# Performance work log

Measured on AMD Instinct MI355X. Metric: run time of the kernel, lower is better.

## Reference

```python
import jax, jax.numpy as jnp
import numpy as np

FIX_SCALE = np.array([[0.,0.,0.],[1.,0.,0.],[0.,1.,0.],[0.,0.,1.],[-1.,0.,0.],[0.,-1.,0.]], dtype=np.float32)
NUM_HEADS = 8
ATTN_DIMS = 512
HEAD_DIMS = ATTN_DIMS // NUM_HEADS
NUM_LEARN = 6
SIG_CLAMP = 9.21  # safe_sigmoid clamp


def quat_to_rotmat(q):
    # q: [G,4] (w,x,y,z), normalized -> [G,3,3]
    q = q / jnp.linalg.norm(q, axis=-1, keepdims=True)
    w, x, y, z = q[..., 0], q[..., 1], q[..., 2], q[..., 3]
    r0 = jnp.stack([1 - 2*(y*y + z*z), 2*(x*y - w*z), 2*(x*z + w*y)], -1)
    r1 = jnp.stack([2*(x*y + w*z), 1 - 2*(x*x + z*z), 2*(y*z - w*x)], -1)
    r2 = jnp.stack([2*(x*z - w*y), 2*(y*z + w*x), 1 - 2*(x*x + y*y)], -1)
    return jnp.stack([r0, r1, r2], -2)


def bilinear_sample(fm, gx, gy):
    # fm: [C,H,W]; gx,gy: [...] in [-1,1]; align_corners=False, zero padding
    C, H, W = fm.shape
    x = (gx + 1.0) * (W * 0.5) - 0.5
    y = (gy + 1.0) * (H * 0.5) - 0.5
    x0 = jnp.floor(x); y0 = jnp.floor(y)
    wx1 = x - x0; wx0 = 1.0 - wx1
    wy1 = y - y0; wy0 = 1.0 - wy1

    def gather(xf, yf):
        xi = xf.astype(jnp.int32); yi = yf.astype(jnp.int32)
        valid = (xi >= 0) & (xi < W) & (yi >= 0) & (yi < H)
        xi = jnp.clip(xi, 0, W - 1); yi = jnp.clip(yi, 0, H - 1)
        return fm[:, yi, xi] * valid[None].astype(fm.dtype)  # [C, ...]

    out = (gather(x0, y0) * (wx0 * wy0)[None]
           + gather(x0 + 1, y0) * (wx1 * wy0)[None]
           + gather(x0, y0 + 1) * (wx0 * wy1)[None]
           + gather(x0 + 1, y0 + 1) * (wx1 * wy1)[None])
    return jnp.moveaxis(out, 0, -1)  # [..., C]


def setup_inputs() -> dict:
    key = jax.random.key(0)
    ks = jax.random.split(key, 16)
    G, BS, GFD = 8192, 1, 32
    means = jax.random.uniform(ks[0], (G, 3), minval=-1.0, maxval=1.0)
    means = means.at[:, 2].add(3.0)  # push in front of camera
    scales = jax.random.uniform(ks[1], (G, 3), minval=0.01, maxval=0.1)
    rotations = jax.random.normal(ks[2], (G, 4))
    features = jax.random.normal(ks[3], (BS, G, 3, GFD))
    transforms = jnp.tile(jnp.eye(4)[None], (G, 1, 1)) + 0.01 * jax.random.normal(ks[4], (G, 4, 4))
    f = 64.0
    proj = jnp.array([[f, 0., 32., 0.], [0., f, 32., 0.], [0., 0., 1., 0.], [0., 0., 0., 1.]], dtype=jnp.float32)
    projection = jnp.tile(proj[None], (BS, 1, 1))
    image_features = jax.random.normal(ks[5], (BS, 256, 64, 64))
    s = lambda d: 1.0 / np.sqrt(d)
    Wq = jax.random.normal(ks[6], (GFD, ATTN_DIMS)) * s(GFD)
    Wk = jax.random.normal(ks[7], (ATTN_DIMS, 256)) * s(256)
    Wv = jax.random.normal(ks[8], (ATTN_DIMS, 256)) * s(256)
    W_off = jax.random.normal(ks[9], (HEAD_DIMS + 3, NUM_LEARN * 3)) * s(HEAD_DIMS + 3)
    b_off = jnp.zeros((NUM_LEARN * 3,))
    Wout = jax.random.normal(ks[10], (ATTN_DIMS, GFD)) * s(ATTN_DIMS)
    b_out = jnp.zeros((GFD,))
    return {"means": means, "scales": scales, "rotations": rotations, "features": features,
            "transforms": transforms, "projection": projection, "image_features": image_features,
            "Wq": Wq, "Wk": Wk, "Wv": Wv, "W_off": W_off, "b_off": b_off, "Wout": Wout, "b_out": b_out}


def reference(means, scales, rotations, features, transforms, projection, image_features,
              Wq, Wk, Wv, W_off, b_off, Wout, b_out):
    G = means.shape[0]
    bs = features.shape[0]
    H, HD = NUM_HEADS, HEAD_DIMS
    h_img, w_img = image_features.shape[-2:]

    # queries: [bs,G,3,attn] -> [bs,H,G,3,hd]
    q_full = jnp.einsum('bgtf,fa->bgta', features, Wq)
    q = q_full.reshape(bs, G, 3, H, HD).transpose(0, 3, 1, 2, 4)

    # transform means to world space with per-gaussian 4x4
    homo = jnp.concatenate([means, jnp.ones((G, 1), means.dtype)], -1)  # [G,4]
    means_w = jnp.einsum('gij,gj->gi', transforms, homo)[:, :3]  # [G,3]

    # OffsetNet: per-head learnable offsets from (world mean, token-mean query)
    q_mean = q.mean(axis=3)  # [bs,H,G,hd]
    m_b = jnp.broadcast_to(means_w[None, None], (bs, H, G, 3))
    off_in = jnp.concatenate([m_b, q_mean], -1)  # [bs,H,G,hd+3]
    learnable = jax.nn.sigmoid(jnp.clip(off_in @ W_off + b_off, -SIG_CLAMP, SIG_CLAMP))
    learnable = learnable.reshape(bs, H, G, NUM_LEARN, 3) - 0.5
    fix = jnp.broadcast_to(jnp.asarray(FIX_SCALE)[None, None, None], (bs, H, G, FIX_SCALE.shape[0], 3))
    scale_all = jnp.concatenate([fix, learnable], axis=-2)  # [bs,H,G,K,3]
    K = scale_all.shape[-2]

    offset_pts = scale_all * scales[None, None, :, None, :]
    RT = jnp.swapaxes(quat_to_rotmat(rotations), -1, -2)  # [G,3,3]
    offset_pts = jnp.einsum('gij,bhgkj->bhgki', RT, offset_pts) + means_w[None, None, :, None, :]

    # project to 2D, normalize to [0,1), then to grid coords [-1,1]
    pts4 = jnp.concatenate([offset_pts, jnp.ones_like(offset_pts[..., :1])], -1)
    p = jnp.einsum('bij,bhgkj->bhgki', projection, pts4)
    p2 = p[..., :2] / jnp.clip(p[..., 2:3], 1e-5)
    wh = jnp.array([w_img, h_img], dtype=p2.dtype)
    pnorm = jnp.clip(p2 / wh, 0.0, 0.9999)
    grid = 2.0 * pnorm - 1.0  # [bs,H,G,K,2]

    # key/value maps via 1x1 conv, split into per-head channel groups
    kmap = jnp.einsum('ac,bchw->bahw', Wk, image_features).reshape(bs, H, HD, h_img, w_img)
    vmap_ = jnp.einsum('ac,bchw->bahw', Wv, image_features).reshape(bs, H, HD, h_img, w_img)

    sample_bh = jax.vmap(jax.vmap(bilinear_sample, in_axes=(0, 0, 0)), in_axes=(0, 0, 0))
    k_s = sample_bh(kmap, grid[..., 0], grid[..., 1])   # [bs,H,G,K,hd]
    v_s = sample_bh(vmap_, grid[..., 0], grid[..., 1])  # [bs,H,G,K,hd]

    scale = HD ** -0.5
    scores = jnp.einsum('bhgid,bhgkd->bhgik', q, k_s) * scale
    attn = jax.nn.softmax(scores, axis=-1)
    out = jnp.einsum('bhgik,bhgkd->bhgid', attn, v_s)  # [bs,H,G,3,hd]
    out = out.transpose(0, 2, 3, 1, 4).reshape(bs, G, 3, H * HD)  # b g i (h d)
    out = out @ Wout + b_out
    return out + features
```

## Files before the change

kernel.cpp:

```cpp
#include <hip/hip_runtime.h>
#include <hip/hip_bf16.h>
#include <hip/hip_fp16.h>

typedef _Float16 half2v __attribute__((ext_vector_type(2)));
typedef _Float16 half8v __attribute__((ext_vector_type(8)));
typedef __attribute__((ext_vector_type(4))) float float4v;

__device__ __forceinline__ half2v u2h(unsigned u) { return __builtin_bit_cast(half2v, u); }
__device__ __forceinline__ unsigned h2u(half2v h) { return __builtin_bit_cast(unsigned, h); }
__device__ __forceinline__ unsigned short f2hu(float f) {
    _Float16 h = (_Float16)f; return __builtin_bit_cast(unsigned short, h);
}
__device__ __forceinline__ unsigned packh(float lo, float hi) {
    half2v h; h[0] = (_Float16)lo; h[1] = (_Float16)hi; return h2u(h);
}
__device__ __forceinline__ void ld8h(const unsigned short* p, float* f) {
    uint4 u = *(const uint4*)p;
    half2v h0 = u2h(u.x), h1 = u2h(u.y), h2 = u2h(u.z), h3 = u2h(u.w);
    f[0] = (float)h0[0]; f[1] = (float)h0[1]; f[2] = (float)h1[0]; f[3] = (float)h1[1];
    f[4] = (float)h2[0]; f[5] = (float)h2[1]; f[6] = (float)h3[0]; f[7] = (float)h3[1];
}

__global__ __launch_bounds__(256) void preconvert_kernel(
    const float* __restrict__ img, const float* __restrict__ Wk,
    const float* __restrict__ Wv, unsigned short* __restrict__ imgh,
    unsigned short* __restrict__ wkvh)
{
    const size_t base = ((size_t)blockIdx.x * 256 + threadIdx.x) * 4;
    float4 v;
    unsigned short* dst;
    if (base < 1048576) {
        v = *(const float4*)(img + base);
        dst = imgh + base;
    } else {
        size_t o = base - 1048576;
        v = *(const float4*)((o < 131072) ? (Wk + o) : (Wv + (o - 131072)));
        dst = wkvh + o;
    }
    *(uint2*)dst = make_uint2(packh(v.x, v.y), packh(v.z, v.w));
}

__global__ __launch_bounds__(256) void conv_f16_kernel(
    const unsigned short* __restrict__ imgh, const unsigned short* __restrict__ wkvh,
    unsigned short* __restrict__ buf)
{
    __shared__ __attribute__((aligned(16))) unsigned short Bt[64][264];
    const int tid = threadIdx.x;
    const int p0 = blockIdx.x * 64;
    const int o0 = blockIdx.y * 64;

#pragma unroll
    for (int i = 0; i < 4; i++) {
        int chunk = i * 256 + tid;
        int kp  = chunk >> 3;
        int pxg = (chunk & 7) * 8;
        uint4 r0 = *(const uint4*)(imgh + (size_t)(2 * kp) * 4096 + p0 + pxg);
        uint4 r1 = *(const uint4*)(imgh + (size_t)(2 * kp + 1) * 4096 + p0 + pxg);
        unsigned lo[8], hi[8];
        lo[0] = r0.x & 0xffffu; lo[1] = r0.x >> 16; lo[2] = r0.y & 0xffffu; lo[3] = r0.y >> 16;
        lo[4] = r0.z & 0xffffu; lo[5] = r0.z >> 16; lo[6] = r0.w & 0xffffu; lo[7] = r0.w >> 16;
        hi[0] = r1.x & 0xffffu; hi[1] = r1.x >> 16; hi[2] = r1.y & 0xffffu; hi[3] = r1.y >> 16;
        hi[4] = r1.z & 0xffffu; hi[5] = r1.z >> 16; hi[6] = r1.w & 0xffffu; hi[7] = r1.w >> 16;
#pragma unroll
        for (int j = 0; j < 8; j++)
            *(unsigned*)&Bt[pxg + j][2 * kp] = lo[j] | (hi[j] << 16);
    }
    __syncthreads();

    const int w = tid >> 6, l = tid & 63;
    const int m = l & 15, quad = l >> 4;
    const int mrow = w * 16 + m;
    const unsigned short* Wsel = wkvh + ((o0 < 512) ? 0 : 131072);
    const int obase = (o0 < 512) ? o0 : (o0 - 512);

    float4v acc[4] = {{0,0,0,0},{0,0,0,0},{0,0,0,0},{0,0,0,0}};
#pragma unroll
    for (int kk = 0; kk < 8; kk++) {
        const int kofs = kk * 32 + quad * 8;
        half8v af = *(const half8v*)&Bt[mrow][kofs];
#pragma unroll
        for (int nt = 0; nt < 4; nt++) {
            const int row = obase + nt * 16 + m;
            half8v b8 = *(const half8v*)(Wsel + (size_t)row * 256 + kofs);
            acc[nt] = __builtin_amdgcn_mfma_f32_16x16x32_f16(af, b8, acc[nt], 0, 0, 0);
        }
    }
#pragma unroll
    for (int nt = 0; nt < 4; nt++) {
#pragma unroll
        for (int r = 0; r < 4; r++) {
            size_t px = p0 + w * 16 + quad * 4 + r;
            buf[px * 1024 + o0 + nt * 16 + m] = f2hu(acc[nt][r]);
        }
    }
}

__global__ __launch_bounds__(256) void conv_mfma_kernel(
    const float* __restrict__ img, const float* __restrict__ Wk,
    const float* __restrict__ Wv, unsigned short* __restrict__ buf)
{
    __shared__ __attribute__((aligned(16))) unsigned short Bt[64][264];
    const int tid = threadIdx.x;
    const int p0 = blockIdx.x * 64;
    const int o0 = blockIdx.y * 64;

#pragma unroll
    for (int i = 0; i < 4; i++) {
        int chunk = i * 256 + tid;
        int kp  = chunk >> 3;
        int pxg = (chunk & 7) * 8;
        const float* r0 = img + (size_t)(2 * kp) * 4096 + p0 + pxg;
        const float* r1 = img + (size_t)(2 * kp + 1) * 4096 + p0 + pxg;
        float4 a0 = *(const float4*)r0, a1 = *(const float4*)(r0 + 4);
        float4 b0 = *(const float4*)r1, b1 = *(const float4*)(r1 + 4);
        unsigned lo[8], hi[8];
        lo[0] = f2hu(a0.x); lo[1] = f2hu(a0.y); lo[2] = f2hu(a0.z); lo[3] = f2hu(a0.w);
        lo[4] = f2hu(a1.x); lo[5] = f2hu(a1.y); lo[6] = f2hu(a1.z); lo[7] = f2hu(a1.w);
        hi[0] = f2hu(b0.x); hi[1] = f2hu(b0.y); hi[2] = f2hu(b0.z); hi[3] = f2hu(b0.w);
        hi[4] = f2hu(b1.x); hi[5] = f2hu(b1.y); hi[6] = f2hu(b1.z); hi[7] = f2hu(b1.w);
#pragma unroll
        for (int j = 0; j < 8; j++)
            *(unsigned*)&Bt[pxg + j][2 * kp] = lo[j] | (hi[j] << 16);
    }
    __syncthreads();

    const int w = tid >> 6, l = tid & 63;
    const int m = l & 15, quad = l >> 4;
    const int mrow = w * 16 + m;
    const float* Wsel = (o0 < 512) ? Wk : Wv;
    const int obase = (o0 < 512) ? o0 : (o0 - 512);

    float4v acc[4] = {{0,0,0,0},{0,0,0,0},{0,0,0,0},{0,0,0,0}};
#pragma unroll
    for (int kk = 0; kk < 8; kk++) {
        const int kofs = kk * 32 + quad * 8;
        half8v af = *(const half8v*)&Bt[mrow][kofs];
#pragma unroll
        for (int nt = 0; nt < 4; nt++) {
            const int row = obase + nt * 16 + m;
            const float* wp = Wsel + (size_t)row * 256 + kofs;
            float4 w0 = *(const float4*)wp, w1 = *(const float4*)(wp + 4);
            half8v b8;
            b8[0] = (_Float16)w0.x; b8[1] = (_Float16)w0.y;
            b8[2] = (_Float16)w0.z; b8[3] = (_Float16)w0.w;
            b8[4] = (_Float16)w1.x; b8[5] = (_Float16)w1.y;
            b8[6] = (_Float16)w1.z; b8[7] = (_Float16)w1.w;
            acc[nt] = __builtin_amdgcn_mfma_f32_16x16x32_f16(af, b8, acc[nt], 0, 0, 0);
        }
    }
#pragma unroll
    for (int nt = 0; nt < 4; nt++) {
#pragma unroll
        for (int r = 0; r < 4; r++) {
            size_t px = p0 + w * 16 + quad * 4 + r;
            buf[px * 1024 + o0 + nt * 16 + m] = f2hu(acc[nt][r]);
        }
    }
}

__global__ __launch_bounds__(256) void qgemm_kernel(
    const float* __restrict__ features, const float* __restrict__ Wq,
    unsigned short* __restrict__ qfull)
{
    __shared__ __attribute__((aligned(16))) unsigned short WqT[256][40];
    const int tid = threadIdx.x;
    const int R0 = blockIdx.x * 64;
    const int n0 = blockIdx.y * 256;
#pragma unroll
    for (int k = 0; k < 32; k++)
        WqT[tid][k] = f2hu(Wq[(size_t)k * 512 + n0 + tid]);
    __syncthreads();

    const int w = tid >> 6, l = tid & 63, m = l & 15, quad = l >> 4;
    const int row = R0 + w * 16 + m;
    const float* fp = features + (size_t)row * 32 + quad * 8;
    float4 f0 = *(const float4*)fp, f1 = *(const float4*)(fp + 4);
    half8v af;
    af[0] = (_Float16)f0.x; af[1] = (_Float16)f0.y;
    af[2] = (_Float16)f0.z; af[3] = (_Float16)f0.w;
    af[4] = (_Float16)f1.x; af[5] = (_Float16)f1.y;
    af[6] = (_Float16)f1.z; af[7] = (_Float16)f1.w;
    float4v acc[16];
#pragma unroll
    for (int t = 0; t < 16; t++) acc[t] = (float4v){0.f, 0.f, 0.f, 0.f};
#pragma unroll
    for (int t = 0; t < 16; t++) {
        half8v b8 = *(const half8v*)&WqT[t * 16 + m][quad * 8];
        acc[t] = __builtin_amdgcn_mfma_f32_16x16x32_f16(af, b8, acc[t], 0, 0, 0);
    }
    const int rb = R0 + w * 16 + quad * 4;
#pragma unroll
    for (int t = 0; t < 16; t++)
#pragma unroll
        for (int r = 0; r < 4; r++)
            qfull[(size_t)(rb + r) * 512 + n0 + t * 16 + m] = f2hu(acc[t][r]);
}

__global__ __launch_bounds__(256, 8) void attn_core_kernel(
    const float* __restrict__ means, const float* __restrict__ scales,
    const float* __restrict__ rot,   const float* __restrict__ transforms,
    const float* __restrict__ projection, const float* __restrict__ W_off,
    const float* __restrict__ b_off, const unsigned short* __restrict__ buf,
    unsigned short* __restrict__ qfull)
{
    __shared__ __attribute__((aligned(16))) unsigned qf2[768];
    __shared__ __attribute__((aligned(16))) unsigned vsh2[3072];
    __shared__ __attribute__((aligned(16))) float qm_u[512];
    __shared__ float lrn[144];
    __shared__ float mw[3], sc3[3], Rt[9], pr[12];

    short4* corner = (short4*)qm_u;
    float*  att    = qm_u + 192;
    float*  wofl   = (float*)vsh2;
    float*  bofl   = wofl + 1206;

    const int g = blockIdx.x, tid = threadIdx.x;

    for (int i = tid; i < 1206; i += 256) wofl[i] = W_off[i];
    if (tid < 18) bofl[tid] = b_off[tid];
    if (tid >= 32 && tid < 35) {
        sc3[tid - 32] = scales[(size_t)g * 3 + (tid - 32)];
    } else if (tid >= 36 && tid < 48) {
        pr[tid - 36] = projection[tid - 36];
    } else if (tid == 48) {
        float w = rot[(size_t)g * 4],     x = rot[(size_t)g * 4 + 1];
        float y = rot[(size_t)g * 4 + 2], z = rot[(size_t)g * 4 + 3];
        float n = rsqrtf(w * w + x * x + y * y + z * z);
        w *= n; x *= n; y *= n; z *= n;
        float R00 = 1 - 2 * (y * y + z * z), R01 = 2 * (x * y - w * z), R02 = 2 * (x * z + w * y);
        float R10 = 2 * (x * y + w * z), R11 = 1 - 2 * (x * x + z * z), R12 = 2 * (y * z - w * x);
        float R20 = 2 * (x * z - w * y), R21 = 2 * (y * z + w * x), R22 = 1 - 2 * (x * x + y * y);
        Rt[0] = R00; Rt[1] = R10; Rt[2] = R20;
        Rt[3] = R01; Rt[4] = R11; Rt[5] = R21;
        Rt[6] = R02; Rt[7] = R12; Rt[8] = R22;
    } else if (tid >= 52 && tid < 55) {
        int i = tid - 52;
        float m0 = means[(size_t)g * 3];
        float m1 = means[(size_t)g * 3 + 1];
        float m2 = means[(size_t)g * 3 + 2];
        const float* T = transforms + (size_t)g * 16 + i * 4;
        mw[i] = T[0] * m0 + T[1] * m1 + T[2] * m2 + T[3];
    }
    {
        const unsigned* qsrc = (const unsigned*)(qfull + (size_t)g * 1536);
#pragma unroll
        for (int i = 0; i < 3; i++) {
            int e = tid + i * 256;
            qf2[e] = qsrc[e];
        }
    }
    __syncthreads();

    {
        half2v a = u2h(qf2[tid]), b = u2h(qf2[256 + tid]), c = u2h(qf2[512 + tid]);
        qm_u[tid * 2]     = ((float)a[0] + (float)b[0] + (float)c[0]) * (1.f / 3.f);
        qm_u[tid * 2 + 1] = ((float)a[1] + (float)b[1] + (float)c[1]) * (1.f / 3.f);
    }
    __syncthreads();

    if (tid < 144) {
        int h = tid / 18, l = tid % 18;
        float s = bofl[l];
#pragma unroll
        for (int i = 0; i < 3; i++) s += mw[i] * wofl[i * 18 + l];
        for (int d = 0; d < 64; d++) s += qm_u[h * 64 + d] * wofl[(3 + d) * 18 + l];
        s = fminf(fmaxf(s, -9.21f), 9.21f);
        lrn[tid] = 1.f / (1.f + expf(-s)) - 0.5f;
    }
    __syncthreads();

    if (tid < 96) {
        int h = tid / 12, k = tid % 12;
        float s0, s1, s2;
        if (k < 6) {
            const float FSx[6] = {0.f, 1.f, 0.f, 0.f, -1.f, 0.f};
            const float FSy[6] = {0.f, 0.f, 1.f, 0.f, 0.f, -1.f};
            const float FSz[6] = {0.f, 0.f, 0.f, 1.f, 0.f, 0.f};
            s0 = FSx[k]; s1 = FSy[k]; s2 = FSz[k];
        } else {
            int b = h * 18 + (k - 6) * 3;
            s0 = lrn[b]; s1 = lrn[b + 1]; s2 = lrn[b + 2];
        }
        float o0 = s0 * sc3[0], o1 = s1 * sc3[1], o2 = s2 * sc3[2];
        float wx = Rt[0] * o0 + Rt[1] * o1 + Rt[2] * o2 + mw[0];
        float wy = Rt[3] * o0 + Rt[4] * o1 + Rt[5] * o2 + mw[1];
        float wz = Rt[6] * o0 + Rt[7] * o1 + Rt[8] * o2 + mw[2];
        float px = pr[0] * wx + pr[1] * wy + pr[2]  * wz + pr[3];
        float py = pr[4] * wx + pr[5] * wy + pr[6]  * wz + pr[7];
        float pz = pr[8] * wx + pr[9] * wy + pr[10] * wz + pr[11];
        pz = fmaxf(pz, 1e-5f);
        float gx = fminf(fmaxf(px / pz * (1.f / 64.f), 0.f), 0.9999f);
        float gy = fminf(fmaxf(py / pz * (1.f / 64.f), 0.f), 0.9999f);
        float x = gx * 64.f - 0.5f, y = gy * 64.f - 0.5f;
        float fx = floorf(x), fy = floorf(y);
        short4 cn;
        cn.x = (short)(int)fx;
        cn.y = (short)(int)fy;
        cn.z = (short)(unsigned short)fminf((x - fx) * 65536.f, 65535.f);
        cn.w = (short)(unsigned short)fminf((y - fy) * 65536.f, 65535.f);
        corner[tid] = cn;
    }
    __syncthreads();

    {
        const int slice = tid & 7, grp = tid >> 3;
#pragma unroll
        for (int it = 0; it < 3; it++) {
            const int p = it * 32 + grp;
            const int h = p / 12, k = p - h * 12;
            short4 cn = corner[p];
            int x0 = cn.x, y0 = cn.y, x1 = x0 + 1, y1 = y0 + 1;
            float wx1 = (float)(unsigned short)cn.z * (1.f / 65536.f);
            float wy1 = (float)(unsigned short)cn.w * (1.f / 65536.f);
            float wx0 = 1.f - wx1, wy0 = 1.f - wy1;
            bool vx0 = (unsigned)x0 < 64u, vx1 = (unsigned)x1 < 64u;
            bool vy0 = (unsigned)y0 < 64u, vy1 = (unsigned)y1 < 64u;
            int xc0 = min(max(x0, 0), 63), xc1 = min(max(x1, 0), 63);
            int yc0 = min(max(y0, 0), 63), yc1 = min(max(y1, 0), 63);
            int   off[4];
            float wt[4];
            off[0] = (yc0 * 64 + xc0) * 1024; wt[0] = (vx0 & vy0) ? wx0 * wy0 : 0.f;
            off[1] = (yc0 * 64 + xc1) * 1024; wt[1] = (vx1 & vy0) ? wx1 * wy0 : 0.f;
            off[2] = (yc1 * 64 + xc0) * 1024; wt[2] = (vx0 & vy1) ? wx0 * wy1 : 0.f;
            off[3] = (yc1 * 64 + xc1) * 1024; wt[3] = (vx1 & vy1) ? wx1 * wy1 : 0.f;
            const int a = h * 64 + slice * 8;
            const unsigned short* bp = buf + a;
            half2v ka2[4] = {{0,0},{0,0},{0,0},{0,0}};
            half2v va2[4] = {{0,0},{0,0},{0,0},{0,0}};
#pragma unroll
            for (int c = 0; c < 4; c++) {
                _Float16 wh = (_Float16)wt[c];
                half2v w2; w2[0] = wh; w2[1] = wh;
                uint4 uk = *(const uint4*)(bp + off[c]);
                uint4 uv = *(const uint4*)(bp + off[c] + 512);
                ka2[0] += w2 * u2h(uk.x); ka2[1] += w2 * u2h(uk.y);
                ka2[2] += w2 * u2h(uk.z); ka2[3] += w2 * u2h(uk.w);
                va2[0] += w2 * u2h(uv.x); va2[1] += w2 * u2h(uv.y);
                va2[2] += w2 * u2h(uv.z); va2[3] += w2 * u2h(uv.w);
            }
            const int pa = h * 32 + slice * 4;
            *(uint4*)&vsh2[p * 32 + slice * 4] =
                make_uint4(h2u(va2[0]), h2u(va2[1]), h2u(va2[2]), h2u(va2[3]));
            float sp[3];
#pragma unroll
            for (int t = 0; t < 3; t++) {
                uint4 q4 = *(const uint4*)&qf2[t * 256 + pa];
                float s = __builtin_amdgcn_fdot2(u2h(q4.x), ka2[0], 0.f, false);
                s = __builtin_amdgcn_fdot2(u2h(q4.y), ka2[1], s, false);
                s = __builtin_amdgcn_fdot2(u2h(q4.z), ka2[2], s, false);
                s = __builtin_amdgcn_fdot2(u2h(q4.w), ka2[3], s, false);
                sp[t] = s;
            }
#pragma unroll
            for (int msk = 1; msk < 8; msk <<= 1) {
#pragma unroll
                for (int t = 0; t < 3; t++) sp[t] += __shfl_xor(sp[t], msk);
            }
            if (slice == 0) {
#pragma unroll
                for (int t = 0; t < 3; t++) att[(h * 3 + t) * 12 + k] = sp[t] * 0.125f;
            }
        }
    }
    __syncthreads();

    if (tid < 24) {
        float* row = att + tid * 12;
        float m = row[0];
#pragma unroll
        for (int k = 1; k < 12; k++) m = fmaxf(m, row[k]);
        float e_[12]; float ssum = 0.f;
#pragma unroll
        for (int k = 0; k < 12; k++) { e_[k] = expf(row[k] - m); ssum += e_[k]; }
        float inv = 1.f / ssum;
#pragma unroll
        for (int k = 0; k < 12; k++) row[k] = e_[k] * inv;
    }
    __syncthreads();

    {
        unsigned* oa32 = (unsigned*)(qfull + (size_t)g * 1536);
#pragma unroll
        for (int i = 0; i < 3; i++) {
            int e = tid + i * 256;
            int t = e >> 8, a2p = e & 255;
            int h = a2p >> 5, ddp = a2p & 31;
            const float* ar = att + (h * 3 + t) * 12;
            const unsigned* vp = vsh2 + h * 12 * 32 + ddp;
            half2v acc = {0, 0};
#pragma unroll
            for (int k = 0; k < 12; k++) {
                _Float16 ah = (_Float16)ar[k];
                half2v a2; a2[0] = ah; a2[1] = ah;
                acc += a2 * u2h(vp[k * 32]);
            }
            oa32[e] = h2u(acc);
        }
    }
}

__global__ __launch_bounds__(256) void outgemm_kernel(
    const unsigned short* __restrict__ oa, const float* __restrict__ Wout,
    const float* __restrict__ b_out, const float* __restrict__ features,
    float* __restrict__ out)
{
    __shared__ __attribute__((aligned(16))) unsigned short WT[32][520];
    const int tid = threadIdx.x;
    const int R0 = blockIdx.x * 64;
#pragma unroll
    for (int j = 0; j < 64; j++) {
        int lin = j * 256 + tid;
        WT[lin & 31][lin >> 5] = f2hu(Wout[lin]);
    }
    __syncthreads();

    const int w = tid >> 6, l = tid & 63, m = l & 15, quad = l >> 4;
    const int row = R0 + w * 16 + m;
    float4v acc[2] = {{0,0,0,0},{0,0,0,0}};
#pragma unroll
    for (int kk = 0; kk < 16; kk++) {
        half8v af = *(const half8v*)(oa + (size_t)row * 512 + kk * 32 + quad * 8);
#pragma unroll
        for (int t = 0; t < 2; t++) {
            half8v b8 = *(const half8v*)&WT[t * 16 + m][kk * 32 + quad * 8];
            acc[t] = __builtin_amdgcn_mfma_f32_16x16x32_f16(af, b8, acc[t], 0, 0, 0);
        }
    }
    const int rb = R0 + w * 16 + quad * 4;
#pragma unroll
    for (int t = 0; t < 2; t++) {
        int col = t * 16 + m;
        float bb = b_out[col];
#pragma unroll
        for (int r = 0; r < 4; r++) {
            int rr = rb + r;
            out[(size_t)rr * 32 + col] = acc[t][r] + bb + features[(size_t)rr * 32 + col];
        }
    }
}

__global__ __launch_bounds__(256, 6) void attn_fused_kernel(
    const float* __restrict__ means, const float* __restrict__ scales,
    const float* __restrict__ rot,   const float* __restrict__ features,
    const float* __restrict__ transforms, const float* __restrict__ projection,
    const float* __restrict__ Wq,    const float* __restrict__ W_off,
    const float* __restrict__ b_off, const float* __restrict__ Wout,
    const float* __restrict__ b_out, const unsigned short* __restrict__ buf,
    float* __restrict__ out)
{
    __shared__ float feat[96];
    __shared__ __attribute__((aligned(16))) float qf[1536];
    __shared__ float qm[512];
    __shared__ float mw[3], sc3[3], Rt[9], pr[12];
    __shared__ float lrn[144];
    __shared__ int   coff[96][4];
    __shared__ float cwt[96][4];
    __shared__ __attribute__((aligned(16))) char pool[12288];
    __shared__ float att[288];

    unsigned short* vsh = (unsigned short*)pool;
    const int g = blockIdx.x, tid = threadIdx.x;

    if (tid < 96) {
        feat[tid] = features[(size_t)g * 96 + tid];
    } else if (tid < 99) {
        sc3[tid - 96] = scales[(size_t)g * 3 + (tid - 96)];
    } else if (tid >= 100 && tid < 112) {
        pr[tid - 100] = projection[tid - 100];
    } else if (tid == 112) {
        float w = rot[(size_t)g * 4],     x = rot[(size_t)g * 4 + 1];
        float y = rot[(size_t)g * 4 + 2], z = rot[(size_t)g * 4 + 3];
        float n = rsqrtf(w * w + x * x + y * y + z * z);
        w *= n; x *= n; y *= n; z *= n;
        float R00 = 1 - 2 * (y * y + z * z), R01 = 2 * (x * y - w * z), R02 = 2 * (x * z + w * y);
        float R10 = 2 * (x * y + w * z), R11 = 1 - 2 * (x * x + z * z), R12 = 2 * (y * z - w * x);
        float R20 = 2 * (x * z - w * y), R21 = 2 * (y * z + w * x), R22 = 1 - 2 * (x * x + y * y);
        Rt[0] = R00; Rt[1] = R10; Rt[2] = R20;
        Rt[3] = R01; Rt[4] = R11; Rt[5] = R21;
        Rt[6] = R02; Rt[7] = R12; Rt[8] = R22;
    } else if (tid >= 116 && tid < 119) {
        int i = tid - 116;
        float m0 = means[(size_t)g * 3];
        float m1 = means[(size_t)g * 3 + 1];
        float m2 = means[(size_t)g * 3 + 2];
        const float* T = transforms + (size_t)g * 16 + i * 4;
        mw[i] = T[0] * m0 + T[1] * m1 + T[2] * m2 + T[3];
    }
    __syncthreads();

    {
        const int a0 = tid * 2;
        float s00 = 0.f, s01 = 0.f, s10 = 0.f, s11 = 0.f, s20 = 0.f, s21 = 0.f;
#pragma unroll
        for (int f = 0; f < 32; f++) {
            float2 w2 = *(const float2*)(Wq + (size_t)f * 512 + a0);
            float f0 = feat[f], f1 = feat[32 + f], f2 = feat[64 + f];
            s00 += f0 * w2.x; s01 += f0 * w2.y;
            s10 += f1 * w2.x; s11 += f1 * w2.y;
            s20 += f2 * w2.x; s21 += f2 * w2.y;
        }
        *(float2*)(qf + a0)        = make_float2(s00, s01);
        *(float2*)(qf + 512 + a0)  = make_float2(s10, s11);
        *(float2*)(qf + 1024 + a0) = make_float2(s20, s21);
    }
    __syncthreads();

    qm[tid]       = (qf[tid]       + qf[tid + 512] + qf[tid + 1024]) * (1.f / 3.f);
    qm[tid + 256] = (qf[tid + 256] + qf[tid + 768] + qf[tid + 1280]) * (1.f / 3.f);
    __syncthreads();

    if (tid < 144) {
        int h = tid / 18, l = tid % 18;
        float s = b_off[l];
#pragma unroll
        for (int i = 0; i < 3; i++) s += mw[i] * W_off[i * 18 + l];
        for (int d = 0; d < 64; d++) s += qm[h * 64 + d] * W_off[(size_t)(3 + d) * 18 + l];
        s = fminf(fmaxf(s, -9.21f), 9.21f);
        lrn[tid] = 1.f / (1.f + expf(-s)) - 0.5f;
    }
    __syncthreads();

    if (tid < 96) {
        int h = tid / 12, k = tid % 12;
        float s0, s1, s2;
        if (k < 6) {
            const float FSx[6] = {0.f, 1.f, 0.f, 0.f, -1.f, 0.f};
            const float FSy[6] = {0.f, 0.f, 1.f, 0.f, 0.f, -1.f};
            const float FSz[6] = {0.f, 0.f, 0.f, 1.f, 0.f, 0.f};
            s0 = FSx[k]; s1 = FSy[k]; s2 = FSz[k];
        } else {
            int b = h * 18 + (k - 6) * 3;
            s0 = lrn[b]; s1 = lrn[b + 1]; s2 = lrn[b + 2];
        }
        float o0 = s0 * sc3[0], o1 = s1 * sc3[1], o2 = s2 * sc3[2];
        float wx = Rt[0] * o0 + Rt[1] * o1 + Rt[2] * o2 + mw[0];
        float wy = Rt[3] * o0 + Rt[4] * o1 + Rt[5] * o2 + mw[1];
        float wz = Rt[6] * o0 + Rt[7] * o1 + Rt[8] * o2 + mw[2];
        float px = pr[0] * wx + pr[1] * wy + pr[2]  * wz + pr[3];
        float py = pr[4] * wx + pr[5] * wy + pr[6]  * wz + pr[7];
        float pz = pr[8] * wx + pr[9] * wy + pr[10] * wz + pr[11];
        pz = fmaxf(pz, 1e-5f);
        float gx = fminf(fmaxf(px / pz * (1.f / 64.f), 0.f), 0.9999f);
        float gy = fminf(fmaxf(py / pz * (1.f / 64.f), 0.f), 0.9999f);
        float x = gx * 64.f - 0.5f, y = gy * 64.f - 0.5f;
        float fx = floorf(x), fy = floorf(y);
        int x0 = (int)fx, y0 = (int)fy;
        float wx1 = x - fx, wx0c = 1.f - wx1;
        float wy1 = y - fy, wy0c = 1.f - wy1;
        int xs[2] = {x0, x0 + 1}, ys[2] = {y0, y0 + 1};
        float wxs[2] = {wx0c, wx1}, wys[2] = {wy0c, wy1};
#pragma unroll
        for (int c = 0; c < 4; c++) {
            int dx = c & 1, dy = c >> 1;
            int xi = xs[dx], yi = ys[dy];
            bool v = (xi >= 0) & (xi < 64) & (yi >= 0) & (yi < 64);
            int xc = min(max(xi, 0), 63), yc = min(max(yi, 0), 63);
            coff[tid][c] = (yc * 64 + xc) * 1024;
            cwt[tid][c]  = v ? wxs[dx] * wys[dy] : 0.f;
        }
    }
    __syncthreads();

    {
        const int slice = tid & 7, d0 = slice * 8, grp = tid >> 3;
#pragma unroll
        for (int it = 0; it < 3; it++) {
            const int p = it * 32 + grp;
            const int h = p / 12, k = p - h * 12;
            const int a = h * 64 + d0;
            const unsigned short* bp = buf + a;
            float ka[8] = {0,0,0,0,0,0,0,0}, va[8] = {0,0,0,0,0,0,0,0}, t8[8];
#pragma unroll
            for (int c = 0; c < 4; c++) {
                const int   o = coff[p][c];
                const float w = cwt[p][c];
                ld8h(bp + o, t8);
#pragma unroll
                for (int j = 0; j < 8; j++) ka[j] += w * t8[j];
                ld8h(bp + o + 512, t8);
#pragma unroll
                for (int j = 0; j < 8; j++) va[j] += w * t8[j];
            }
            uint4 pv;
            pv.x = packh(va[0], va[1]); pv.y = packh(va[2], va[3]);
            pv.z = packh(va[4], va[5]); pv.w = packh(va[6], va[7]);
            *(uint4*)(vsh + p * 64 + d0) = pv;
            float sp[3];
#pragma unroll
            for (int t = 0; t < 3; t++) {
                const float* qp = qf + t * 512 + a;
                float s = 0.f;
#pragma unroll
                for (int j = 0; j < 8; j++) s += qp[j] * ka[j];
                sp[t] = s;
            }
#pragma unroll
            for (int msk = 1; msk < 8; msk <<= 1) {
#pragma unroll
                for (int t = 0; t < 3; t++) sp[t] += __shfl_xor(sp[t], msk);
            }
            if (slice == 0) {
#pragma unroll
                for (int t = 0; t < 3; t++) att[(h * 3 + t) * 12 + k] = sp[t] * 0.125f;
            }
        }
    }
    __syncthreads();

    if (tid < 24) {
        float* row = att + tid * 12;
        float m = row[0];
#pragma unroll
        for (int k = 1; k < 12; k++) m = fmaxf(m, row[k]);
        float e_[12]; float ssum = 0.f;
#pragma unroll
        for (int k = 0; k < 12; k++) { e_[k] = expf(row[k] - m); ssum += e_[k]; }
        float inv = 1.f / ssum;
#pragma unroll
        for (int k = 0; k < 12; k++) row[k] = e_[k] * inv;
    }
    __syncthreads();

#pragma unroll
    for (int i = 0; i < 6; i++) {
        int e = tid + i * 256;
        int t = e >> 9, a = e & 511, h = a >> 6, dd = a & 63;
        const float* ar = att + (h * 3 + t) * 12;
        const unsigned short* vp = vsh + (h * 12) * 64 + dd;
        float s = 0.f;
#pragma unroll
        for (int k = 0; k < 12; k++) {
            _Float16 hh = __builtin_bit_cast(_Float16, vp[k * 64]);
            s += ar[k] * (float)hh;
        }
        qf[e] = s;
    }
    __syncthreads();

    {
        float* red = (float*)pool;
        const int c0 = (tid & 15) * 2, slice = tid >> 4;
        const int abase = slice * 32;
        float a00 = 0.f, a01 = 0.f, a10 = 0.f, a11 = 0.f, a20 = 0.f, a21 = 0.f;
#pragma unroll
        for (int i = 0; i < 32; i++) {
            int a = abase + i;
            float2 w2 = *(const float2*)(Wout + (size_t)a * 32 + c0);
            float o0 = qf[a], o1 = qf[512 + a], o2 = qf[1024 + a];
            a00 += o0 * w2.x; a01 += o0 * w2.y;
            a10 += o1 * w2.x; a11 += o1 * w2.y;
            a20 += o2 * w2.x; a21 += o2 * w2.y;
        }
        __syncthreads();
        red[(slice * 3 + 0) * 32 + c0] = a00; red[(slice * 3 + 0) * 32 + c0 + 1] = a01;
        red[(slice * 3 + 1) * 32 + c0] = a10; red[(slice * 3 + 1) * 32 + c0 + 1] = a11;
        red[(slice * 3 + 2) * 32 + c0] = a20; red[(slice * 3 + 2) * 32 + c0 + 1] = a21;
        __syncthreads();
        if (tid < 96) {
            int t = tid >> 5, c = tid & 31;
            float acc = b_out[c] + feat[tid];
#pragma unroll
            for (int s = 0; s < 16; s++) acc += red[(s * 3 + t) * 32 + c];
            out[(size_t)g * 96 + tid] = acc;
        }
    }
}

extern "C" void kernel_launch(void* const* d_in, const int* in_sizes, int n_in,
                              void* d_out, int out_size, void* d_ws, size_t ws_size,
                              hipStream_t stream) {
    const float* means      = (const float*)d_in[0];
    const float* scales     = (const float*)d_in[1];
    const float* rot        = (const float*)d_in[2];
    const float* features   = (const float*)d_in[3];
    const float* transforms = (const float*)d_in[4];
    const float* projection = (const float*)d_in[5];
    const float* img        = (const float*)d_in[6];
    const float* Wq         = (const float*)d_in[7];
    const float* Wk         = (const float*)d_in[8];
    const float* Wv         = (const float*)d_in[9];
    const float* W_off      = (const float*)d_in[10];
    const float* b_off      = (const float*)d_in[11];
    const float* Wout       = (const float*)d_in[12];
    const float* b_out      = (const float*)d_in[13];
    float* out = (float*)d_out;

    char* w = (char*)d_ws;
    unsigned short* buf = (unsigned short*)(w + 64);
    const size_t BUF_BYTES = (size_t)4096 * 1024 * 2;
    const size_t Q_BYTES   = (size_t)24576 * 512 * 2;
    const size_t need = 64 + BUF_BYTES + Q_BYTES;

    dim3 gridc(64, 16);
    if (ws_size >= need) {
        unsigned short* qfull = (unsigned short*)(w + 64 + BUF_BYTES);
        unsigned short* imgh = qfull;
        unsigned short* wkvh = imgh + 1048576;
        preconvert_kernel<<<1280, 256, 0, stream>>>(img, Wk, Wv, imgh, wkvh);
        conv_f16_kernel<<<gridc, 256, 0, stream>>>(imgh, wkvh, buf);
        dim3 gridq(384, 2);
        qgemm_kernel<<<gridq, 256, 0, stream>>>(features, Wq, qfull);
        attn_core_kernel<<<8192, 256, 0, stream>>>(
            means, scales, rot, transforms, projection, W_off, b_off, buf, qfull);
        outgemm_kernel<<<384, 256, 0, stream>>>(qfull, Wout, b_out, features, out);
    } else {
        conv_mfma_kernel<<<gridc, 256, 0, stream>>>(img, Wk, Wv, buf);
        attn_fused_kernel<<<8192, 256, 0, stream>>>(
            means, scales, rot, features, transforms, projection,
            Wq, W_off, b_off, Wout, b_out, buf, out);
    }
}
```

Before: 174.5 us.

## Fuse fp16 conversion into conv kernel, stage weights in LDS, batch gather loads

```diff
diff --git a/kernel.cpp b/kernel.cpp
--- a/kernel.cpp
+++ b/kernel.cpp
@@ -21,88 +21,17 @@
     f[4] = (float)h2[0]; f[5] = (float)h2[1]; f[6] = (float)h3[0]; f[7] = (float)h3[1];
 }
 
-__global__ __launch_bounds__(256) void preconvert_kernel(
-    const float* __restrict__ img, const float* __restrict__ Wk,
-    const float* __restrict__ Wv, unsigned short* __restrict__ imgh,
-    unsigned short* __restrict__ wkvh)
-{
-    const size_t base = ((size_t)blockIdx.x * 256 + threadIdx.x) * 4;
-    float4 v;
-    unsigned short* dst;
-    if (base < 1048576) {
-        v = *(const float4*)(img + base);
-        dst = imgh + base;
-    } else {
-        size_t o = base - 1048576;
-        v = *(const float4*)((o < 131072) ? (Wk + o) : (Wv + (o - 131072)));
-        dst = wkvh + o;
-    }
-    *(uint2*)dst = make_uint2(packh(v.x, v.y), packh(v.z, v.w));
-}
-
-__global__ __launch_bounds__(256) void conv_f16_kernel(
-    const unsigned short* __restrict__ imgh, const unsigned short* __restrict__ wkvh,
-    unsigned short* __restrict__ buf)
-{
-    __shared__ __attribute__((aligned(16))) unsigned short Bt[64][264];
-    const int tid = threadIdx.x;
-    const int p0 = blockIdx.x * 64;
-    const int o0 = blockIdx.y * 64;
-
-#pragma unroll
-    for (int i = 0; i < 4; i++) {
-        int chunk = i * 256 + tid;
-        int kp  = chunk >> 3;
-        int pxg = (chunk & 7) * 8;
-        uint4 r0 = *(const uint4*)(imgh + (size_t)(2 * kp) * 4096 + p0 + pxg);
-        uint4 r1 = *(const uint4*)(imgh + (size_t)(2 * kp + 1) * 4096 + p0 + pxg);
-        unsigned lo[8], hi[8];
-        lo[0] = r0.x & 0xffffu; lo[1] = r0.x >> 16; lo[2] = r0.y & 0xffffu; lo[3] = r0.y >> 16;
-        lo[4] = r0.z & 0xffffu; lo[5] = r0.z >> 16; lo[6] = r0.w & 0xffffu; lo[7] = r0.w >> 16;
-        hi[0] = r1.x & 0xffffu; hi[1] = r1.x >> 16; hi[2] = r1.y & 0xffffu; hi[3] = r1.y >> 16;
-        hi[4] = r1.z & 0xffffu; hi[5] = r1.z >> 16; hi[6] = r1.w & 0xffffu; hi[7] = r1.w >> 16;
-#pragma unroll
-        for (int j = 0; j < 8; j++)
-            *(unsigned*)&Bt[pxg + j][2 * kp] = lo[j] | (hi[j] << 16);
-    }
-    __syncthreads();
-
-    const int w = tid >> 6, l = tid & 63;
-    const int m = l & 15, quad = l >> 4;
-    const int mrow = w * 16 + m;
-    const unsigned short* Wsel = wkvh + ((o0 < 512) ? 0 : 131072);
-    const int obase = (o0 < 512) ? o0 : (o0 - 512);
-
-    float4v acc[4] = {{0,0,0,0},{0,0,0,0},{0,0,0,0},{0,0,0,0}};
-#pragma unroll
-    for (int kk = 0; kk < 8; kk++) {
-        const int kofs = kk * 32 + quad * 8;
-        half8v af = *(const half8v*)&Bt[mrow][kofs];
-#pragma unroll
-        for (int nt = 0; nt < 4; nt++) {
-            const int row = obase + nt * 16 + m;
-            half8v b8 = *(const half8v*)(Wsel + (size_t)row * 256 + kofs);
-            acc[nt] = __builtin_amdgcn_mfma_f32_16x16x32_f16(af, b8, acc[nt], 0, 0, 0);
-        }
-    }
-#pragma unroll
-    for (int nt = 0; nt < 4; nt++) {
-#pragma unroll
-        for (int r = 0; r < 4; r++) {
-            size_t px = p0 + w * 16 + quad * 4 + r;
-            buf[px * 1024 + o0 + nt * 16 + m] = f2hu(acc[nt][r]);
-        }
-    }
-}
-
-__global__ __launch_bounds__(256) void conv_mfma_kernel(
+__global__ __launch_bounds__(256) void conv_fused_kernel(
     const float* __restrict__ img, const float* __restrict__ Wk,
     const float* __restrict__ Wv, unsigned short* __restrict__ buf)
 {
     __shared__ __attribute__((aligned(16))) unsigned short Bt[64][264];
+    __shared__ __attribute__((aligned(16))) unsigned short Wt[64][264];
     const int tid = threadIdx.x;
     const int p0 = blockIdx.x * 64;
     const int o0 = blockIdx.y * 64;
+    const float* Wsel = (o0 < 512) ? Wk : Wv;
+    const int obase = (o0 < 512) ? o0 : (o0 - 512);
 
 #pragma unroll
     for (int i = 0; i < 4; i++) {
@@ -122,13 +51,24 @@
         for (int j = 0; j < 8; j++)
             *(unsigned*)&Bt[pxg + j][2 * kp] = lo[j] | (hi[j] << 16);
     }
+    {
+        const int row = tid >> 2, q = tid & 3;
+        const float* wp = Wsel + (size_t)(obase + row) * 256 + q * 64;
+#pragma unroll
+        for (int j = 0; j < 8; j++) {
+            float4 w0 = *(const float4*)(wp + j * 8);
+            float4 w1 = *(const float4*)(wp + j * 8 + 4);
+            uint4 pk;
+            pk.x = packh(w0.x, w0.y); pk.y = packh(w0.z, w0.w);
+            pk.z = packh(w1.x, w1.y); pk.w = packh(w1.z, w1.w);
+            *(uint4*)&Wt[row][q * 64 + j * 8] = pk;
+        }
+    }
     __syncthreads();
 
     const int w = tid >> 6, l = tid & 63;
     const int m = l & 15, quad = l >> 4;
     const int mrow = w * 16 + m;
-    const float* Wsel = (o0 < 512) ? Wk : Wv;
-    const int obase = (o0 < 512) ? o0 : (o0 - 512);
 
     float4v acc[4] = {{0,0,0,0},{0,0,0,0},{0,0,0,0},{0,0,0,0}};
 #pragma unroll
@@ -137,14 +77,7 @@
         half8v af = *(const half8v*)&Bt[mrow][kofs];
 #pragma unroll
         for (int nt = 0; nt < 4; nt++) {
-            const int row = obase + nt * 16 + m;
-            const float* wp = Wsel + (size_t)row * 256 + kofs;
-            float4 w0 = *(const float4*)wp, w1 = *(const float4*)(wp + 4);
-            half8v b8;
-            b8[0] = (_Float16)w0.x; b8[1] = (_Float16)w0.y;
-            b8[2] = (_Float16)w0.z; b8[3] = (_Float16)w0.w;
-            b8[4] = (_Float16)w1.x; b8[5] = (_Float16)w1.y;
-            b8[6] = (_Float16)w1.z; b8[7] = (_Float16)w1.w;
+            half8v b8 = *(const half8v*)&Wt[nt * 16 + m][kofs];
             acc[nt] = __builtin_amdgcn_mfma_f32_16x16x32_f16(af, b8, acc[nt], 0, 0, 0);
         }
     }
@@ -196,7 +129,7 @@
             qfull[(size_t)(rb + r) * 512 + n0 + t * 16 + m] = f2hu(acc[t][r]);
 }
 
-__global__ __launch_bounds__(256, 8) void attn_core_kernel(
+__global__ __launch_bounds__(256, 6) void attn_core_kernel(
     const float* __restrict__ means, const float* __restrict__ scales,
     const float* __restrict__ rot,   const float* __restrict__ transforms,
     const float* __restrict__ projection, const float* __restrict__ W_off,
@@ -325,18 +258,22 @@
             off[3] = (yc1 * 64 + xc1) * 1024; wt[3] = (vx1 & vy1) ? wx1 * wy1 : 0.f;
             const int a = h * 64 + slice * 8;
             const unsigned short* bp = buf + a;
+            uint4 uk[4], uv[4];
+#pragma unroll
+            for (int c = 0; c < 4; c++) {
+                uk[c] = *(const uint4*)(bp + off[c]);
+                uv[c] = *(const uint4*)(bp + off[c] + 512);
+            }
             half2v ka2[4] = {{0,0},{0,0},{0,0},{0,0}};
             half2v va2[4] = {{0,0},{0,0},{0,0},{0,0}};
 #pragma unroll
             for (int c = 0; c < 4; c++) {
                 _Float16 wh = (_Float16)wt[c];
                 half2v w2; w2[0] = wh; w2[1] = wh;
-                uint4 uk = *(const uint4*)(bp + off[c]);
-                uint4 uv = *(const uint4*)(bp + off[c] + 512);
-                ka2[0] += w2 * u2h(uk.x); ka2[1] += w2 * u2h(uk.y);
-                ka2[2] += w2 * u2h(uk.z); ka2[3] += w2 * u2h(uk.w);
-                va2[0] += w2 * u2h(uv.x); va2[1] += w2 * u2h(uv.y);
-                va2[2] += w2 * u2h(uv.z); va2[3] += w2 * u2h(uv.w);
+                ka2[0] += w2 * u2h(uk[c].x); ka2[1] += w2 * u2h(uk[c].y);
+                ka2[2] += w2 * u2h(uk[c].z); ka2[3] += w2 * u2h(uk[c].w);
+                va2[0] += w2 * u2h(uv[c].x); va2[1] += w2 * u2h(uv[c].y);
+                va2[2] += w2 * u2h(uv[c].z); va2[3] += w2 * u2h(uv[c].w);
             }
             const int pa = h * 32 + slice * 4;
             *(uint4*)&vsh2[p * 32 + slice * 4] =
@@ -692,19 +629,16 @@
     const size_t need = 64 + BUF_BYTES + Q_BYTES;
 
     dim3 gridc(64, 16);
+    conv_fused_kernel<<<gridc, 256, 0, stream>>>(img, Wk, Wv, buf);
+
     if (ws_size >= need) {
         unsigned short* qfull = (unsigned short*)(w + 64 + BUF_BYTES);
-        unsigned short* imgh = qfull;
-        unsigned short* wkvh = imgh + 1048576;
-        preconvert_kernel<<<1280, 256, 0, stream>>>(img, Wk, Wv, imgh, wkvh);
-        conv_f16_kernel<<<gridc, 256, 0, stream>>>(imgh, wkvh, buf);
         dim3 gridq(384, 2);
         qgemm_kernel<<<gridq, 256, 0, stream>>>(features, Wq, qfull);
         attn_core_kernel<<<8192, 256, 0, stream>>>(
             means, scales, rot, transforms, projection, W_off, b_off, buf, qfull);
         outgemm_kernel<<<384, 256, 0, stream>>>(qfull, Wout, b_out, features, out);
     } else {
-        conv_mfma_kernel<<<gridc, 256, 0, stream>>>(img, Wk, Wv, buf);
         attn_fused_kernel<<<8192, 256, 0, stream>>>(
             means, scales, rot, features, transforms, projection,
             Wq, W_off, b_off, Wout, b_out, buf, out);
```

After: 165.3 us (median of 2 runs). -5.3%, faster.
